# Performance work log

Measured on AMD Instinct MI355X. Metric: run time of the kernel, lower is better.

Reference implementation:

```python
import jax, jax.numpy as jnp
import numpy as np

L, H, LATENT, DM, DH, FF = 4, 4, 256, 768, 192, 1024
EPS = 1e-6      # fast_transformers RecurrentLinearAttention eps
LN_EPS = 1e-5


def make_pe(d_model=LATENT, max_len=5000):
    pos = np.arange(max_len, dtype=np.float32)[:, None]
    div = np.exp(np.arange(0, d_model, 2, dtype=np.float32) * (-np.log(10000.0) / d_model))
    pe = np.zeros((max_len, d_model), np.float32)
    pe[:, 0::2] = np.sin(pos * div)
    pe[:, 1::2] = np.cos(pos * div)
    return jnp.asarray(pe)

PE = make_pe()


def layer_norm(x, g, b):
    m = x.mean(-1, keepdims=True)
    v = ((x - m) ** 2).mean(-1, keepdims=True)
    return (x - m) * jax.lax.rsqrt(v + LN_EPS) * g + b


def setup_inputs() -> dict:
    key = jax.random.key(0)
    ks = jax.random.split(key, 16)
    bs, nj, nf, T, A, C = 8, 25, 6, 80, 6, 12
    s = 0.02
    return dict(
        x=jax.random.normal(ks[0], (bs, nj, nf, T), jnp.float32),
        y=jax.random.randint(ks[1], (bs, A), 0, C),
        ind_map=jnp.sort(jax.random.randint(ks[2], (T, bs), 0, A), axis=0),
        act_tstamps=jnp.sort(jax.random.randint(ks[3], (bs, A), 1, T + 1), axis=1).at[:, -1].set(T),
        skel_W=jax.random.normal(ks[4], (nj * nf, LATENT), jnp.float32) * s,
        skel_b=jnp.zeros((LATENT,), jnp.float32),
        muQuery=jax.random.normal(ks[5], (C, LATENT), jnp.float32),
        sigmaQuery=jax.random.normal(ks[6], (C, LATENT), jnp.float32),
        Wq=jax.random.normal(ks[7], (L, DM, DM), jnp.float32) * s,
        bq=jnp.zeros((L, DM), jnp.float32),
        Wk=jax.random.normal(ks[8], (L, DM, DM), jnp.float32) * s,
        bk=jnp.zeros((L, DM), jnp.float32),
        Wv=jax.random.normal(ks[9], (L, DM, DM), jnp.float32) * s,
        bv=jnp.zeros((L, DM), jnp.float32),
        Wo=jax.random.normal(ks[10], (L, DM, DM), jnp.float32) * s,
        bo=jnp.zeros((L, DM), jnp.float32),
        W1=jax.random.normal(ks[11], (L, DM, FF), jnp.float32) * s,
        b1=jnp.zeros((L, FF), jnp.float32),
        W2=jax.random.normal(ks[12], (L, FF, DM), jnp.float32) * s,
        b2=jnp.zeros((L, DM), jnp.float32),
        ln1_g=jnp.ones((L, DM), jnp.float32), ln1_b=jnp.zeros((L, DM), jnp.float32),
        ln2_g=jnp.ones((L, DM), jnp.float32), ln2_b=jnp.zeros((L, DM), jnp.float32),
        lnf_g=jnp.ones((DM,), jnp.float32), lnf_b=jnp.zeros((DM,), jnp.float32),
    )


def _fwd(x, y, ind_map, act_tstamps, skel_W, skel_b, muQuery, sigmaQuery,
         Wq, bq, Wk, bk, Wv, bv, Wo, bo, W1, b1, W2, b2,
         ln1_g, ln1_b, ln2_g, ln2_b, lnf_g, lnf_b):
    bs, nj, nf, T = x.shape
    # skeleton embedding: [T, bs, njoints*nfeats] @ W -> [T, bs, LATENT]
    xe = x.transpose(3, 0, 1, 2).reshape(T, bs, nj * nf) @ skel_W + skel_b
    mu_q = muQuery[y]        # [bs, A, LATENT]
    sig_q = sigmaQuery[y]
    barange = jnp.arange(bs)

    @jax.checkpoint
    def step(carry, inputs):
        S, Z = carry                         # [L,bs,H,DH,DH], [L,bs,H,DH]
        t, xt, ind_t = inputs
        cm = mu_q[barange, ind_t]            # gather per-sample current action query
        cs = sig_q[barange, ind_t]
        xseq = jnp.stack([cm, cs, xt], 0)    # [3, bs, LATENT]
        start = jnp.where(t == 0, 0, t + 2)  # PositionalEncoding(last_pos=t, offset=2)
        pe3 = jax.lax.dynamic_slice_in_dim(PE, start, 3, 0)
        xseq = xseq + pe3[:, None, :]
        h = xseq.transpose(1, 0, 2).reshape(bs, 3 * LATENT)  # flatten -> [bs, DM]
        nS, nZ = [], []
        for l in range(L):
            q = (h @ Wq[l] + bq[l]).reshape(bs, H, DH)
            k = (h @ Wk[l] + bk[l]).reshape(bs, H, DH)
            v = (h @ Wv[l] + bv[l]).reshape(bs, H, DH)
            Q = jax.nn.elu(q) + 1.0          # linear-attention feature map
            K = jax.nn.elu(k) + 1.0
            Sl = S[l] + K[..., :, None] * v[..., None, :]   # state update S += k (x) v
            Zl = Z[l] + K
            inv = 1.0 / (jnp.einsum('bhd,bhd->bh', Q, Zl) + EPS)
            att = jnp.einsum('bhd,bhdm,bh->bhm', Q, Sl, inv).reshape(bs, DM)
            h1 = layer_norm(h + att @ Wo[l] + bo[l], ln1_g[l], ln1_b[l])
            ffn = jax.nn.relu(h1 @ W1[l] + b1[l]) @ W2[l] + b2[l]
            h = layer_norm(h1 + ffn, ln2_g[l], ln2_b[l])
            nS.append(Sl); nZ.append(Zl)
        h = layer_norm(h, lnf_g, lnf_b)      # encoder final norm
        return (jnp.stack(nS), jnp.stack(nZ)), h

    S0 = jnp.zeros((L, bs, H, DH, DH), x.dtype)
    Z0 = jnp.zeros((L, bs, H, DH), x.dtype)
    _, finals = jax.lax.scan(step, (S0, Z0), (jnp.arange(T), xe, ind_map))  # finals: [T,bs,DM]
    tsel = jnp.maximum(act_tstamps - 1, 0)                       # [bs, A]
    mu = finals[:, :, :LATENT][tsel, barange[:, None]]           # [bs, A, LATENT]
    logvar = finals[:, :, LATENT:2 * LATENT][tsel, barange[:, None]]
    return mu, logvar


def reference(x, y, ind_map, act_tstamps, skel_W, skel_b, muQuery, sigmaQuery,
              Wq, bq, Wk, bk, Wv, bv, Wo, bo, W1, b1, W2, b2,
              ln1_g, ln1_b, ln2_g, ln2_b, lnf_g, lnf_b):
    return _fwd(x, y, ind_map, act_tstamps, skel_W, skel_b, muQuery, sigmaQuery,
                Wq, bq, Wk, bk, Wv, bv, Wo, bo, W1, b1, W2, b2,
                ln1_g, ln1_b, ln2_g, ln2_b, lnf_g, lnf_b)
```

## Files before the change

kernel.cpp:

```cpp
#include <hip/hip_runtime.h>
#include <math.h>

#define TT 80
#define BS 8
#define NA 6
#define DMODEL 768
#define NH 4
#define DH 192
#define FFD 1024
#define NROWS (TT*BS)
#define NQKV (3*DMODEL)

typedef __bf16 bf16;
typedef __bf16 bf16x8 __attribute__((ext_vector_type(8)));
typedef float  f32x4  __attribute__((ext_vector_type(4)));

__device__ __forceinline__ float block_reduce_sum256(float v, float* sm4) {
#pragma unroll
    for (int off = 32; off > 0; off >>= 1) v += __shfl_down(v, off, 64);
    int lane = threadIdx.x & 63, wid = threadIdx.x >> 6;
    if (lane == 0) sm4[wid] = v;
    __syncthreads();
    float r = sm4[0] + sm4[1] + sm4[2] + sm4[3];
    __syncthreads();
    return r;
}

__global__ __launch_bounds__(256) void embed_k(
        const float* __restrict__ x, const int* __restrict__ y,
        const int* __restrict__ ind_map, const float* __restrict__ skel_W,
        const float* __restrict__ skel_b, const float* __restrict__ muQ,
        const float* __restrict__ sigQ, float* __restrict__ h0,
        bf16* __restrict__ h0b) {
    __shared__ float xrow[152];
    int r = blockIdx.x;
    int t = r >> 3, b = r & 7;
    int c = threadIdx.x;
    if (c < 150) xrow[c] = x[(b * 150 + c) * TT + t];
    __syncthreads();
    float acc = skel_b[c];
    for (int jf = 0; jf < 150; jf++) acc += xrow[jf] * skel_W[jf * 256 + c];
    int ind_t = ind_map[t * 8 + b];
    int yb = y[b * NA + ind_t];
    float cm = muQ[yb * 256 + c];
    float cs = sigQ[yb * 256 + c];
    int start = (t == 0) ? 0 : (t + 2);
    float div = expf((float)(c & ~1) * (-9.210340371976184f / 256.0f));
    float p0, p1, p2;
    if (c & 1) {
        p0 = cosf((float)start * div);
        p1 = cosf((float)(start + 1) * div);
        p2 = cosf((float)(start + 2) * div);
    } else {
        p0 = sinf((float)start * div);
        p1 = sinf((float)(start + 1) * div);
        p2 = sinf((float)(start + 2) * div);
    }
    float* hr = h0 + (size_t)r * DMODEL;
    float v0 = cm + p0, v1 = cs + p1, v2 = acc + p2;
    hr[c] = v0; hr[c + 256] = v1; hr[c + 512] = v2;
    bf16* hb = h0b + (size_t)r * DMODEL;
    hb[c] = (bf16)v0; hb[c + 256] = (bf16)v1; hb[c + 512] = (bf16)v2;
}

__global__ __launch_bounds__(256) void transpose_k(
        const float* __restrict__ Wq, const float* __restrict__ Wk,
        const float* __restrict__ Wv, const float* __restrict__ Wo,
        const float* __restrict__ W1, const float* __restrict__ W2,
        bf16* __restrict__ qkvT, bf16* __restrict__ woT,
        bf16* __restrict__ w1T, bf16* __restrict__ w2T) {
    int lz = blockIdx.z;
    int l = lz >> 2, z = lz & 3;
    int K = (z == 3) ? 1024 : 768;
    int N = (z == 0) ? 2304 : (z == 2) ? 1024 : 768;
    int k0 = blockIdx.x * 32, n0 = blockIdx.y * 32;
    if (k0 >= K || n0 >= N) return;
    const float* src; bf16* dst; int ldsrc; int ncol;
    if (z == 0) {
        if (n0 < 768)       { src = Wq + (size_t)l * 768 * 768; ncol = n0; }
        else if (n0 < 1536) { src = Wk + (size_t)l * 768 * 768; ncol = n0 - 768; }
        else                { src = Wv + (size_t)l * 768 * 768; ncol = n0 - 1536; }
        dst = qkvT + (size_t)l * NQKV * DMODEL; ldsrc = 768;
    } else if (z == 1) { src = Wo + (size_t)l * 768 * 768;  dst = woT + (size_t)l * 768 * 768;  ldsrc = 768;  ncol = n0; }
    else if (z == 2)   { src = W1 + (size_t)l * 768 * 1024; dst = w1T + (size_t)l * 1024 * 768; ldsrc = 1024; ncol = n0; }
    else               { src = W2 + (size_t)l * 1024 * 768; dst = w2T + (size_t)l * 768 * 1024; ldsrc = 768;  ncol = n0; }
    __shared__ float tile[32][33];
    int tx = threadIdx.x & 31, ty = threadIdx.x >> 5;
#pragma unroll
    for (int i = 0; i < 4; i++) {
        int r = ty + 8 * i;
        tile[r][tx] = src[(size_t)(k0 + r) * ldsrc + ncol + tx];
    }
    __syncthreads();
#pragma unroll
    for (int i = 0; i < 4; i++) {
        int r = ty + 8 * i;
        dst[(size_t)(n0 + r) * K + k0 + tx] = (bf16)tile[tx][r];
    }
}

template <int EPI>
__global__ __launch_bounds__(256) void gemm_mfma(
        const bf16* __restrict__ A, const bf16* __restrict__ Bt,
        const float* __restrict__ bias_q, const float* __restrict__ bias_k,
        const float* __restrict__ bias_v, const float* __restrict__ resid,
        float* __restrict__ outF, bf16* __restrict__ outB,
        int M, int N, int K) {
    __shared__ __attribute__((aligned(16))) bf16 As0[64][40];
    __shared__ __attribute__((aligned(16))) bf16 As1[64][40];
    __shared__ __attribute__((aligned(16))) bf16 Bs0[64][40];
    __shared__ __attribute__((aligned(16))) bf16 Bs1[64][40];
    int tid = threadIdx.x;
    int m0 = blockIdx.y * 64, n0 = blockIdx.x * 64;
    int w = tid >> 6;
    int l = tid & 63;
    int lm = l & 15, lq = l >> 4;
    int sr = tid >> 2;
    int sk = (tid & 3) * 8;
    const bf16* Arow = &A[(size_t)(m0 + sr) * K];
    const bf16* Brow = &Bt[(size_t)(n0 + sr) * K];
    f32x4 acc[4] = {};
    uint4 a0 = *(const uint4*)&Arow[sk];
    uint4 a1 = *(const uint4*)&Arow[32 + sk];
    uint4 b0 = *(const uint4*)&Brow[sk];
    uint4 b1 = *(const uint4*)&Brow[32 + sk];
    for (int k0 = 0; k0 < K; k0 += 64) {
        __syncthreads();
        *(uint4*)&As0[sr][sk] = a0;
        *(uint4*)&As1[sr][sk] = a1;
        *(uint4*)&Bs0[sr][sk] = b0;
        *(uint4*)&Bs1[sr][sk] = b1;
        __syncthreads();
        int k2 = k0 + 64; if (k2 >= K) k2 = 0;
        a0 = *(const uint4*)&Arow[k2 + sk];
        a1 = *(const uint4*)&Arow[k2 + 32 + sk];
        b0 = *(const uint4*)&Brow[k2 + sk];
        b1 = *(const uint4*)&Brow[k2 + 32 + sk];
        bf16x8 af0 = *(bf16x8*)&As0[w * 16 + lm][lq * 8];
        bf16x8 af1 = *(bf16x8*)&As1[w * 16 + lm][lq * 8];
#pragma unroll
        for (int nb = 0; nb < 4; nb++) {
            bf16x8 bf0 = *(bf16x8*)&Bs0[nb * 16 + lm][lq * 8];
            acc[nb] = __builtin_amdgcn_mfma_f32_16x16x32_bf16(af0, bf0, acc[nb], 0, 0, 0);
        }
#pragma unroll
        for (int nb = 0; nb < 4; nb++) {
            bf16x8 bf1 = *(bf16x8*)&Bs1[nb * 16 + lm][lq * 8];
            acc[nb] = __builtin_amdgcn_mfma_f32_16x16x32_bf16(af1, bf1, acc[nb], 0, 0, 0);
        }
    }
#pragma unroll
    for (int nb = 0; nb < 4; nb++) {
        int col = n0 + nb * 16 + lm;
        float b;
        bool do_elu = false;
        if (EPI == 0) {
            if (col < 768)       { b = bias_q[col];        do_elu = true; }
            else if (col < 1536) { b = bias_k[col - 768];  do_elu = true; }
            else                 { b = bias_v[col - 1536]; }
        } else {
            b = bias_q[col];
        }
#pragma unroll
        for (int r = 0; r < 4; r++) {
            int row = m0 + w * 16 + lq * 4 + r;
            float v = acc[nb][r] + b;
            if (EPI == 0) {
                if (do_elu) v = (v > 0.0f) ? (v + 1.0f) : expf(v);
                outB[(size_t)row * N + col] = (bf16)v;
            } else if (EPI == 1) {
                v += resid[(size_t)row * N + col];
                outF[(size_t)row * N + col] = v;
            } else {
                v = fmaxf(v, 0.0f);
                outB[(size_t)row * N + col] = (bf16)v;
            }
        }
    }
}

__global__ __launch_bounds__(256) void ln_k(
        const float* __restrict__ in, float* __restrict__ outF,
        bf16* __restrict__ outB,
        const float* __restrict__ g, const float* __restrict__ b) {
    int wave = threadIdx.x >> 6, lane = threadIdx.x & 63;
    int row = blockIdx.x * 4 + wave;
    const float* xr = in + (size_t)row * DMODEL;
    float4 v[3];
    float s = 0.0f;
#pragma unroll
    for (int j = 0; j < 3; j++) {
        v[j] = *(const float4*)&xr[lane * 4 + 256 * j];
        s += v[j].x + v[j].y + v[j].z + v[j].w;
    }
#pragma unroll
    for (int mk = 1; mk < 64; mk <<= 1) s += __shfl_xor(s, mk, 64);
    float m = s * (1.0f / 768.0f);
    float sq = 0.0f;
#pragma unroll
    for (int j = 0; j < 3; j++) {
        v[j].x -= m; v[j].y -= m; v[j].z -= m; v[j].w -= m;
        sq += v[j].x * v[j].x + v[j].y * v[j].y + v[j].z * v[j].z + v[j].w * v[j].w;
    }
#pragma unroll
    for (int mk = 1; mk < 64; mk <<= 1) sq += __shfl_xor(sq, mk, 64);
    float r = rsqrtf(sq * (1.0f / 768.0f) + 1e-5f);
    float* orow = outF + (size_t)row * DMODEL;
    bf16* brow = outB + (size_t)row * DMODEL;
#pragma unroll
    for (int j = 0; j < 3; j++) {
        int c = lane * 4 + 256 * j;
        float4 gg = *(const float4*)&g[c];
        float4 bb = *(const float4*)&b[c];
        float o0 = v[j].x * r * gg.x + bb.x;
        float o1 = v[j].y * r * gg.y + bb.y;
        float o2 = v[j].z * r * gg.z + bb.z;
        float o3 = v[j].w * r * gg.w + bb.w;
        *(float4*)&orow[c] = make_float4(o0, o1, o2, o3);
        bf16 tmp4[4] = {(bf16)o0, (bf16)o1, (bf16)o2, (bf16)o3};
        *(uint2*)&brow[c] = *(uint2*)tmp4;
    }
}

__global__ __launch_bounds__(320) void attn_k(
        const bf16* __restrict__ qkvB, bf16* __restrict__ att) {
    __shared__ __attribute__((aligned(16))) char smem[64000];
    bf16* Qs = (bf16*)smem;
    bf16* Ks = (bf16*)(smem + 32000);
    bf16* Aij = (bf16*)smem;
    bf16* VT = (bf16*)(smem + 16640);

    int b = blockIdx.x >> 2, h = blockIdx.x & 3;
    int tid = threadIdx.x;
    int w = tid >> 6, l = tid & 63;
    int lm = l & 15, lq = l >> 4;

    uint4 vreg[6];
#pragma unroll
    for (int u = 0; u < 6; u++) {
        int c = tid + 320 * u;
        int t = c / 24, cc = c % 24;
        int d0 = cc * 8;
        size_t g = (size_t)(t * 8 + b) * NQKV + h * DH + d0;
        uint4 qv = *(const uint4*)&qkvB[g];
        uint4 kv = *(const uint4*)&qkvB[g + 768];
        vreg[u]  = *(const uint4*)&qkvB[g + 1536];
        *(uint4*)&Qs[t * 200 + d0] = qv;
        *(uint4*)&Ks[t * 200 + d0] = kv;
    }
    __syncthreads();

    f32x4 acc[5] = {};
#pragma unroll
    for (int k0 = 0; k0 < 192; k0 += 32) {
        bf16x8 af = *(bf16x8*)&Qs[(w * 16 + lm) * 200 + lq * 8 + k0];
#pragma unroll
        for (int nb = 0; nb < 5; nb++) {
            bf16x8 bfr = *(bf16x8*)&Ks[(nb * 16 + lm) * 200 + lq * 8 + k0];
            acc[nb] = __builtin_amdgcn_mfma_f32_16x16x32_bf16(af, bfr, acc[nb], 0, 0, 0);
        }
    }
    float mval[5][4];
    float rs[4] = {0.f, 0.f, 0.f, 0.f};
#pragma unroll
    for (int nb = 0; nb < 5; nb++)
#pragma unroll
        for (int r = 0; r < 4; r++) {
            int t = w * 16 + lq * 4 + r, tau = nb * 16 + lm;
            float v = (tau <= t) ? acc[nb][r] : 0.0f;
            mval[nb][r] = v;
            rs[r] += v;
        }
#pragma unroll
    for (int mk = 1; mk < 16; mk <<= 1)
#pragma unroll
        for (int r = 0; r < 4; r++) rs[r] += __shfl_xor(rs[r], mk, 64);
    float inv[4];
#pragma unroll
    for (int r = 0; r < 4; r++) inv[r] = 1.0f / (rs[r] + 1e-6f);

    __syncthreads();

#pragma unroll
    for (int nb = 0; nb < 5; nb++)
#pragma unroll
        for (int r = 0; r < 4; r++)
            Aij[(w * 16 + lq * 4 + r) * 104 + nb * 16 + lm] = (bf16)mval[nb][r];
    *(uint2*)&Aij[(tid >> 2) * 104 + 80 + (tid & 3) * 4] = make_uint2(0u, 0u);
#pragma unroll
    for (int u = 0; u < 6; u++) {
        int c = tid + 320 * u;
        int t = c / 24, cc = c % 24;
        int d0 = cc * 8;
        bf16 tmp8[8];
        *(uint4*)tmp8 = vreg[u];
#pragma unroll
        for (int j = 0; j < 8; j++) VT[(d0 + j) * 104 + t] = tmp8[j];
    }
    if (tid < 192) {
        *(uint4*)&VT[tid * 104 + 80] = make_uint4(0u, 0u, 0u, 0u);
        *(uint4*)&VT[tid * 104 + 88] = make_uint4(0u, 0u, 0u, 0u);
    }
    __syncthreads();

#pragma unroll 1
    for (int nc = 0; nc < 12; nc++) {
        f32x4 a2 = {};
#pragma unroll
        for (int k0 = 0; k0 < 96; k0 += 32) {
            bf16x8 af = *(bf16x8*)&Aij[(w * 16 + lm) * 104 + lq * 8 + k0];
            bf16x8 bfr = *(bf16x8*)&VT[(nc * 16 + lm) * 104 + lq * 8 + k0];
            a2 = __builtin_amdgcn_mfma_f32_16x16x32_bf16(af, bfr, a2, 0, 0, 0);
        }
#pragma unroll
        for (int r = 0; r < 4; r++) {
            int t = w * 16 + lq * 4 + r;
            att[(size_t)(t * 8 + b) * DMODEL + h * DH + nc * 16 + lm] =
                (bf16)(a2[r] * inv[r]);
        }
    }
}

__global__ __launch_bounds__(256) void final_k(
        const float* __restrict__ h, const int* __restrict__ act_ts,
        const float* __restrict__ g, const float* __restrict__ bb,
        float* __restrict__ out) {
    __shared__ float sm4[4];
    int ba = blockIdx.x;
    int b = ba / NA;
    int ts = act_ts[ba];
    int t = ts - 1; if (t < 0) t = 0;
    const float* xr = h + (size_t)(t * 8 + b) * DMODEL;
    int c = threadIdx.x;
    float x0 = xr[c], x1 = xr[c + 256], x2 = xr[c + 512];
    float m = block_reduce_sum256(x0 + x1 + x2, sm4) * (1.0f / 768.0f);
    float d0 = x0 - m, d1 = x1 - m, d2 = x2 - m;
    float v = block_reduce_sum256(d0 * d0 + d1 * d1 + d2 * d2, sm4) * (1.0f / 768.0f);
    float r = rsqrtf(v + 1e-5f);
    out[ba * 256 + c]            = d0 * r * g[c] + bb[c];
    out[48 * 256 + ba * 256 + c] = d1 * r * g[c + 256] + bb[c + 256];
}

extern "C" void kernel_launch(void* const* d_in, const int* in_sizes, int n_in,
                              void* d_out, int out_size, void* d_ws, size_t ws_size,
                              hipStream_t stream) {
    const float* x       = (const float*)d_in[0];
    const int*   y       = (const int*)d_in[1];
    const int*   ind_map = (const int*)d_in[2];
    const int*   act_ts  = (const int*)d_in[3];
    const float* skel_W  = (const float*)d_in[4];
    const float* skel_b  = (const float*)d_in[5];
    const float* muQ     = (const float*)d_in[6];
    const float* sigQ    = (const float*)d_in[7];
    const float* Wq = (const float*)d_in[8];   const float* bq = (const float*)d_in[9];
    const float* Wk = (const float*)d_in[10];  const float* bk = (const float*)d_in[11];
    const float* Wv = (const float*)d_in[12];  const float* bv = (const float*)d_in[13];
    const float* Wo = (const float*)d_in[14];  const float* bo = (const float*)d_in[15];
    const float* W1 = (const float*)d_in[16];  const float* b1 = (const float*)d_in[17];
    const float* W2 = (const float*)d_in[18];  const float* b2 = (const float*)d_in[19];
    const float* ln1_g = (const float*)d_in[20]; const float* ln1_b = (const float*)d_in[21];
    const float* ln2_g = (const float*)d_in[22]; const float* ln2_b = (const float*)d_in[23];
    const float* lnf_g = (const float*)d_in[24]; const float* lnf_b = (const float*)d_in[25];
    float* out = (float*)d_out;

    char* p = (char*)d_ws;
    const size_t R  = (size_t)NROWS * DMODEL;
    float* h    = (float*)p; p += R * 4;
    float* h1   = (float*)p; p += R * 4;
    float* tmp  = (float*)p; p += R * 4;
    bf16* qkvB  = (bf16*)p;  p += (size_t)NROWS * NQKV * 2;
    bf16* hB    = (bf16*)p;  p += R * 2;
    bf16* h1B   = (bf16*)p;  p += R * 2;
    bf16* attB  = (bf16*)p;  p += R * 2;
    bf16* ffn1B = (bf16*)p;  p += (size_t)NROWS * FFD * 2;
    bf16* qkvT  = (bf16*)p;  p += (size_t)4 * NQKV * DMODEL * 2;
    bf16* woT   = (bf16*)p;  p += (size_t)4 * DMODEL * DMODEL * 2;
    bf16* w1T   = (bf16*)p;  p += (size_t)4 * FFD * DMODEL * 2;
    bf16* w2T   = (bf16*)p;  p += (size_t)4 * DMODEL * FFD * 2;

    dim3 gT(32, 72, 16);
    transpose_k<<<gT, 256, 0, stream>>>(Wq, Wk, Wv, Wo, W1, W2, qkvT, woT, w1T, w2T);
    embed_k<<<NROWS, 256, 0, stream>>>(x, y, ind_map, skel_W, skel_b, muQ, sigQ, h, hB);

    dim3 gQKV(NQKV / 64, 10);
    dim3 g768(12, 10);
    dim3 g1024(16, 10);
    for (int l = 0; l < 4; l++) {
        const bf16* qkvTl = qkvT + (size_t)l * NQKV * DMODEL;
        const bf16* woTl  = woT  + (size_t)l * DMODEL * DMODEL;
        const bf16* w1Tl  = w1T  + (size_t)l * FFD * DMODEL;
        const bf16* w2Tl  = w2T  + (size_t)l * DMODEL * FFD;
        gemm_mfma<0><<<gQKV, 256, 0, stream>>>(hB, qkvTl,
                bq + l * DMODEL, bk + l * DMODEL, bv + l * DMODEL,
                nullptr, nullptr, qkvB, NROWS, NQKV, DMODEL);
        attn_k<<<32, 320, 0, stream>>>(qkvB, attB);
        gemm_mfma<1><<<g768, 256, 0, stream>>>(attB, woTl,
                bo + l * DMODEL, nullptr, nullptr, h, tmp, nullptr,
                NROWS, DMODEL, DMODEL);
        ln_k<<<NROWS / 4, 256, 0, stream>>>(tmp, h1, h1B, ln1_g + l * DMODEL, ln1_b + l * DMODEL);
        gemm_mfma<2><<<g1024, 256, 0, stream>>>(h1B, w1Tl,
                b1 + l * FFD, nullptr, nullptr, nullptr, nullptr, ffn1B,
                NROWS, FFD, DMODEL);
        gemm_mfma<1><<<g768, 256, 0, stream>>>(ffn1B, w2Tl,
                b2 + l * DMODEL, nullptr, nullptr, h1, tmp, nullptr,
                NROWS, DMODEL, FFD);
        ln_k<<<NROWS / 4, 256, 0, stream>>>(tmp, h, hB, ln2_g + l * DMODEL, ln2_b + l * DMODEL);
    }

    final_k<<<48, 256, 0, stream>>>(h, act_ts, lnf_g, lnf_b, out);
}
```

Before: 423.6 us.

## Fuse LayerNorm into GEMM prologue/epilogue via atomic row stats; merge prep kernels

Removes the standalone LayerNorm kernels. The residual GEMM epilogue now accumulates each row's sum and sum-of-squares with atomics, and the next GEMM normalizes its fp32 A operand on the fly, or normalizes the residual in its epilogue. The weight transpose and embedding are merged into one prep kernel that also zeroes the stats buffer. Attention is split across three blocks per batch-head to raise parallelism. This trades fewer launches and fewer round trips to memory for fp32 A loads in the fused GEMMs, a single-pass variance formula that is less numerically stable, and duplicated QK work in attention.

After: 441.2 us. 4.1% more time.

```diff
diff --git a/kernel.cpp b/kernel.cpp
--- a/kernel.cpp
+++ b/kernel.cpp
@@ -5,15 +5,368 @@
 #define BS 8
 #define NA 6
 #define DMODEL 768
-#define NH 4
 #define DH 192
 #define FFD 1024
-#define NROWS (TT*BS)
-#define NQKV (3*DMODEL)
+#define NROWS 640
+#define NQKV 2304
 
 typedef __bf16 bf16;
 typedef __bf16 bf16x8 __attribute__((ext_vector_type(8)));
 typedef float  f32x4  __attribute__((ext_vector_type(4)));
+
+__device__ __forceinline__ void row_ms(const float* __restrict__ st, int row,
+                                       float& m, float& rs) {
+    float s1 = st[row * 2], s2 = st[row * 2 + 1];
+    m = s1 * (1.0f / 768.0f);
+    float var = s2 * (1.0f / 768.0f) - m * m;
+    rs = rsqrtf(var + 1e-5f);
+}
+
+struct TJob { const float* src; bf16* dst; int ldsrc, Kd, n0, k0; };
+
+__global__ __launch_bounds__(256) void prep_k(
+        const float* __restrict__ x, const int* __restrict__ y,
+        const int* __restrict__ ind_map,
+        const float* __restrict__ skel_W, const float* __restrict__ skel_b,
+        const float* __restrict__ muQ, const float* __restrict__ sigQ,
+        const float* __restrict__ Wq, const float* __restrict__ Wk,
+        const float* __restrict__ Wv, const float* __restrict__ Wo,
+        const float* __restrict__ W1, const float* __restrict__ W2,
+        bf16* __restrict__ qkvT, bf16* __restrict__ woT,
+        bf16* __restrict__ w1T, bf16* __restrict__ w2T,
+        float* __restrict__ h, bf16* __restrict__ h0B,
+        float* __restrict__ stats) {
+    __shared__ float tile[32][33];
+    __shared__ float xrow[152];
+    int bid = blockIdx.x, tid = threadIdx.x;
+    if (bid < 15360) {
+        TJob J;
+        int l = bid / 3840, r = bid % 3840;
+        if (r < 1728) {
+            int kt = r % 24, nt = r / 24;
+            J.k0 = kt * 32; J.n0 = nt * 32; J.Kd = 768; J.ldsrc = 768;
+            J.dst = qkvT + (size_t)l * NQKV * DMODEL;
+            if (J.n0 < 768)       { J.src = Wq + (size_t)l * 589824 + J.n0; }
+            else if (J.n0 < 1536) { J.src = Wk + (size_t)l * 589824 + (J.n0 - 768); }
+            else                  { J.src = Wv + (size_t)l * 589824 + (J.n0 - 1536); }
+        } else if (r < 2304) {
+            int r2 = r - 1728; int kt = r2 % 24, nt = r2 / 24;
+            J.k0 = kt * 32; J.n0 = nt * 32; J.Kd = 768; J.ldsrc = 768;
+            J.src = Wo + (size_t)l * 589824 + J.n0;
+            J.dst = woT + (size_t)l * 589824;
+        } else if (r < 3072) {
+            int r2 = r - 2304; int kt = r2 % 24, nt = r2 / 24;
+            J.k0 = kt * 32; J.n0 = nt * 32; J.Kd = 768; J.ldsrc = 1024;
+            J.src = W1 + (size_t)l * 786432 + J.n0;
+            J.dst = w1T + (size_t)l * 786432;
+        } else {
+            int r2 = r - 3072; int kt = r2 % 32, nt = r2 / 32;
+            J.k0 = kt * 32; J.n0 = nt * 32; J.Kd = 1024; J.ldsrc = 768;
+            J.src = W2 + (size_t)l * 786432 + J.n0;
+            J.dst = w2T + (size_t)l * 786432;
+        }
+        int tx = tid & 31, ty = tid >> 5;
+#pragma unroll
+        for (int i = 0; i < 4; i++) {
+            int rr = ty + 8 * i;
+            tile[rr][tx] = J.src[(size_t)(J.k0 + rr) * J.ldsrc + tx];
+        }
+        __syncthreads();
+#pragma unroll
+        for (int i = 0; i < 4; i++) {
+            int rr = ty + 8 * i;
+            J.dst[(size_t)(J.n0 + rr) * J.Kd + J.k0 + tx] = (bf16)tile[tx][rr];
+        }
+    } else {
+        int r = bid - 15360;
+        int t = r >> 3, b = r & 7;
+        int c = tid;
+        if (c < 16) {
+            int arr = c >> 3, l = (c >> 1) & 3, j = c & 1;
+            stats[arr * 5120 + l * 1280 + r * 2 + j] = 0.0f;
+        }
+        if (c < 150) xrow[c] = x[(b * 150 + c) * TT + t];
+        __syncthreads();
+        float acc = skel_b[c];
+        for (int jf = 0; jf < 150; jf++) acc += xrow[jf] * skel_W[jf * 256 + c];
+        int ind_t = ind_map[t * 8 + b];
+        int yb = y[b * NA + ind_t];
+        float cm = muQ[yb * 256 + c];
+        float cs = sigQ[yb * 256 + c];
+        int start = (t == 0) ? 0 : (t + 2);
+        float div = expf((float)(c & ~1) * (-9.210340371976184f / 256.0f));
+        float p0, p1, p2;
+        if (c & 1) {
+            p0 = cosf((float)start * div);
+            p1 = cosf((float)(start + 1) * div);
+            p2 = cosf((float)(start + 2) * div);
+        } else {
+            p0 = sinf((float)start * div);
+            p1 = sinf((float)(start + 1) * div);
+            p2 = sinf((float)(start + 2) * div);
+        }
+        float* hr = h + (size_t)r * DMODEL;
+        float v0 = cm + p0, v1 = cs + p1, v2 = acc + p2;
+        hr[c] = v0; hr[c + 256] = v1; hr[c + 512] = v2;
+        bf16* hb = h0B + (size_t)r * DMODEL;
+        hb[c] = (bf16)v0; hb[c + 256] = (bf16)v1; hb[c + 512] = (bf16)v2;
+    }
+}
+
+template <int EPI, int ANORM, int RNORM>
+__global__ __launch_bounds__(256) void gemm_mfma(
+        const bf16* __restrict__ Ab, const float* __restrict__ Af,
+        const float* __restrict__ stA, const float* __restrict__ gA,
+        const float* __restrict__ bA,
+        const bf16* __restrict__ Bt,
+        const float* __restrict__ bias_q, const float* __restrict__ bias_k,
+        const float* __restrict__ bias_v,
+        const float* __restrict__ residF, const float* __restrict__ stR,
+        const float* __restrict__ gR, const float* __restrict__ bR,
+        float* __restrict__ outF, bf16* __restrict__ outB,
+        float* __restrict__ stOut, int N, int K) {
+    __shared__ __attribute__((aligned(16))) bf16 As0[64][40];
+    __shared__ __attribute__((aligned(16))) bf16 As1[64][40];
+    __shared__ __attribute__((aligned(16))) bf16 Bs0[64][40];
+    __shared__ __attribute__((aligned(16))) bf16 Bs1[64][40];
+    int tid = threadIdx.x;
+    int m0 = blockIdx.y * 64, n0 = blockIdx.x * 64;
+    int w = tid >> 6, l = tid & 63;
+    int lm = l & 15, lq = l >> 4;
+    int sr = tid >> 2;
+    int sk = (tid & 3) * 8;
+    int arow = m0 + sr;
+    const bf16* Brow = &Bt[(size_t)(n0 + sr) * K];
+    f32x4 acc[4] = {};
+    const bf16* Abrow = nullptr; const float* Afrow = nullptr;
+    float mA = 0.f, rsA = 0.f;
+    if (ANORM) {
+        Afrow = &Af[(size_t)arow * K];
+        row_ms(stA, arow, mA, rsA);
+    } else {
+        Abrow = &Ab[(size_t)arow * K];
+    }
+    uint4 a0, a1;
+    f32x4 ax0a, ax0b, ax1a, ax1b;
+    if (ANORM) {
+        ax0a = *(const f32x4*)&Afrow[sk];      ax0b = *(const f32x4*)&Afrow[sk + 4];
+        ax1a = *(const f32x4*)&Afrow[32 + sk]; ax1b = *(const f32x4*)&Afrow[36 + sk];
+    } else {
+        a0 = *(const uint4*)&Abrow[sk];
+        a1 = *(const uint4*)&Abrow[32 + sk];
+    }
+    uint4 b0 = *(const uint4*)&Brow[sk];
+    uint4 b1 = *(const uint4*)&Brow[32 + sk];
+    for (int k0 = 0; k0 < K; k0 += 64) {
+        __syncthreads();
+        if (ANORM) {
+            union { bf16 t[8]; uint4 u; } c0, c1;
+            const float* gp = gA + k0 + sk;
+            const float* bp = bA + k0 + sk;
+#pragma unroll
+            for (int j = 0; j < 4; j++) {
+                c0.t[j]     = (bf16)((ax0a[j] - mA) * rsA * gp[j]      + bp[j]);
+                c0.t[j + 4] = (bf16)((ax0b[j] - mA) * rsA * gp[j + 4]  + bp[j + 4]);
+                c1.t[j]     = (bf16)((ax1a[j] - mA) * rsA * gp[32 + j] + bp[32 + j]);
+                c1.t[j + 4] = (bf16)((ax1b[j] - mA) * rsA * gp[36 + j] + bp[36 + j]);
+            }
+            *(uint4*)&As0[sr][sk] = c0.u;
+            *(uint4*)&As1[sr][sk] = c1.u;
+        } else {
+            *(uint4*)&As0[sr][sk] = a0;
+            *(uint4*)&As1[sr][sk] = a1;
+        }
+        *(uint4*)&Bs0[sr][sk] = b0;
+        *(uint4*)&Bs1[sr][sk] = b1;
+        __syncthreads();
+        int k2 = k0 + 64; if (k2 >= K) k2 = 0;
+        if (ANORM) {
+            ax0a = *(const f32x4*)&Afrow[k2 + sk];      ax0b = *(const f32x4*)&Afrow[k2 + sk + 4];
+            ax1a = *(const f32x4*)&Afrow[k2 + 32 + sk]; ax1b = *(const f32x4*)&Afrow[k2 + 36 + sk];
+        } else {
+            a0 = *(const uint4*)&Abrow[k2 + sk];
+            a1 = *(const uint4*)&Abrow[k2 + 32 + sk];
+        }
+        b0 = *(const uint4*)&Brow[k2 + sk];
+        b1 = *(const uint4*)&Brow[k2 + 32 + sk];
+        bf16x8 af0 = *(bf16x8*)&As0[w * 16 + lm][lq * 8];
+        bf16x8 af1 = *(bf16x8*)&As1[w * 16 + lm][lq * 8];
+#pragma unroll
+        for (int nb = 0; nb < 4; nb++) {
+            bf16x8 bfr = *(bf16x8*)&Bs0[nb * 16 + lm][lq * 8];
+            acc[nb] = __builtin_amdgcn_mfma_f32_16x16x32_bf16(af0, bfr, acc[nb], 0, 0, 0);
+        }
+#pragma unroll
+        for (int nb = 0; nb < 4; nb++) {
+            bf16x8 bfr = *(bf16x8*)&Bs1[nb * 16 + lm][lq * 8];
+            acc[nb] = __builtin_amdgcn_mfma_f32_16x16x32_bf16(af1, bfr, acc[nb], 0, 0, 0);
+        }
+    }
+    if (EPI == 1) {
+        float mR4[4], rsR4[4];
+        if (RNORM) {
+#pragma unroll
+            for (int r = 0; r < 4; r++)
+                row_ms(stR, m0 + w * 16 + lq * 4 + r, mR4[r], rsR4[r]);
+        }
+        float s1[4] = {0.f, 0.f, 0.f, 0.f}, s2[4] = {0.f, 0.f, 0.f, 0.f};
+#pragma unroll
+        for (int nb = 0; nb < 4; nb++) {
+            int col = n0 + nb * 16 + lm;
+            float bia = bias_q[col];
+            float gc = 0.f, bc = 0.f;
+            if (RNORM) { gc = gR[col]; bc = bR[col]; }
+#pragma unroll
+            for (int r = 0; r < 4; r++) {
+                int row = m0 + w * 16 + lq * 4 + r;
+                float rv = residF[(size_t)row * N + col];
+                if (RNORM) rv = (rv - mR4[r]) * rsR4[r] * gc + bc;
+                float v = acc[nb][r] + bia + rv;
+                outF[(size_t)row * N + col] = v;
+                s1[r] += v; s2[r] += v * v;
+            }
+        }
+#pragma unroll
+        for (int mk = 1; mk < 16; mk <<= 1) {
+#pragma unroll
+            for (int r = 0; r < 4; r++) {
+                s1[r] += __shfl_xor(s1[r], mk, 64);
+                s2[r] += __shfl_xor(s2[r], mk, 64);
+            }
+        }
+        if (lm == 0) {
+#pragma unroll
+            for (int r = 0; r < 4; r++) {
+                int row = m0 + w * 16 + lq * 4 + r;
+                atomicAdd(&stOut[row * 2],     s1[r]);
+                atomicAdd(&stOut[row * 2 + 1], s2[r]);
+            }
+        }
+    } else {
+#pragma unroll
+        for (int nb = 0; nb < 4; nb++) {
+            int col = n0 + nb * 16 + lm;
+            float bia; bool do_elu = false;
+            if (EPI == 0) {
+                if (col < 768)       { bia = bias_q[col];        do_elu = true; }
+                else if (col < 1536) { bia = bias_k[col - 768];  do_elu = true; }
+                else                 { bia = bias_v[col - 1536]; }
+            } else {
+                bia = bias_q[col];
+            }
+#pragma unroll
+            for (int r = 0; r < 4; r++) {
+                int row = m0 + w * 16 + lq * 4 + r;
+                float v = acc[nb][r] + bia;
+                if (EPI == 0) {
+                    if (do_elu) v = (v > 0.0f) ? (v + 1.0f) : expf(v);
+                    outB[(size_t)row * N + col] = (bf16)v;
+                } else {
+                    outB[(size_t)row * N + col] = (bf16)fmaxf(v, 0.0f);
+                }
+            }
+        }
+    }
+}
+
+__global__ __launch_bounds__(320) void attn_k(
+        const bf16* __restrict__ qkvB, bf16* __restrict__ att) {
+    __shared__ __attribute__((aligned(16))) char smem[64000];
+    bf16* Qs = (bf16*)smem;
+    bf16* Ks = (bf16*)(smem + 32000);
+    bf16* Aij = (bf16*)smem;
+    bf16* VT = (bf16*)(smem + 16640);
+    int bh = blockIdx.x / 3, part = blockIdx.x % 3;
+    int bb = bh >> 2, hd = bh & 3;
+    int tid = threadIdx.x;
+    int w = tid >> 6, l = tid & 63;
+    int lm = l & 15, lq = l >> 4;
+
+    uint4 vreg[6];
+#pragma unroll
+    for (int u = 0; u < 6; u++) {
+        int c = tid + 320 * u;
+        int t = c / 24, cc = c % 24;
+        int d0 = cc * 8;
+        size_t g = (size_t)(t * 8 + bb) * NQKV + hd * DH + d0;
+        uint4 qv = *(const uint4*)&qkvB[g];
+        uint4 kv = *(const uint4*)&qkvB[g + 768];
+        vreg[u]  = *(const uint4*)&qkvB[g + 1536];
+        *(uint4*)&Qs[t * 200 + d0] = qv;
+        *(uint4*)&Ks[t * 200 + d0] = kv;
+    }
+    __syncthreads();
+
+    f32x4 acc[5] = {};
+#pragma unroll
+    for (int k0 = 0; k0 < 192; k0 += 32) {
+        bf16x8 af = *(bf16x8*)&Qs[(w * 16 + lm) * 200 + lq * 8 + k0];
+#pragma unroll
+        for (int nb = 0; nb < 5; nb++) {
+            bf16x8 bfr = *(bf16x8*)&Ks[(nb * 16 + lm) * 200 + lq * 8 + k0];
+            acc[nb] = __builtin_amdgcn_mfma_f32_16x16x32_bf16(af, bfr, acc[nb], 0, 0, 0);
+        }
+    }
+    float mval[5][4];
+    float rs[4] = {0.f, 0.f, 0.f, 0.f};
+#pragma unroll
+    for (int nb = 0; nb < 5; nb++)
+#pragma unroll
+        for (int r = 0; r < 4; r++) {
+            int t = w * 16 + lq * 4 + r, tau = nb * 16 + lm;
+            float v = (tau <= t) ? acc[nb][r] : 0.0f;
+            mval[nb][r] = v;
+            rs[r] += v;
+        }
+#pragma unroll
+    for (int mk = 1; mk < 16; mk <<= 1)
+#pragma unroll
+        for (int r = 0; r < 4; r++) rs[r] += __shfl_xor(rs[r], mk, 64);
+    float inv[4];
+#pragma unroll
+    for (int r = 0; r < 4; r++) inv[r] = 1.0f / (rs[r] + 1e-6f);
+
+    __syncthreads();
+
+#pragma unroll
+    for (int nb = 0; nb < 5; nb++)
+#pragma unroll
+        for (int r = 0; r < 4; r++)
+            Aij[(w * 16 + lq * 4 + r) * 104 + nb * 16 + lm] = (bf16)mval[nb][r];
+    *(uint2*)&Aij[(tid >> 2) * 104 + 80 + (tid & 3) * 4] = make_uint2(0u, 0u);
+#pragma unroll
+    for (int u = 0; u < 6; u++) {
+        int c = tid + 320 * u;
+        int t = c / 24, cc = c % 24;
+        int d0 = cc * 8;
+        bf16 tmp8[8];
+        *(uint4*)tmp8 = vreg[u];
+#pragma unroll
+        for (int j = 0; j < 8; j++) VT[(d0 + j) * 104 + t] = tmp8[j];
+    }
+    if (tid < 192) {
+        *(uint4*)&VT[tid * 104 + 80] = make_uint4(0u, 0u, 0u, 0u);
+        *(uint4*)&VT[tid * 104 + 88] = make_uint4(0u, 0u, 0u, 0u);
+    }
+    __syncthreads();
+
+#pragma unroll 1
+    for (int nc = part * 4; nc < part * 4 + 4; nc++) {
+        f32x4 a2 = {};
+#pragma unroll
+        for (int k0 = 0; k0 < 96; k0 += 32) {
+            bf16x8 af = *(bf16x8*)&Aij[(w * 16 + lm) * 104 + lq * 8 + k0];
+            bf16x8 bfr = *(bf16x8*)&VT[(nc * 16 + lm) * 104 + lq * 8 + k0];
+            a2 = __builtin_amdgcn_mfma_f32_16x16x32_bf16(af, bfr, a2, 0, 0, 0);
+        }
+#pragma unroll
+        for (int r = 0; r < 4; r++) {
+            int t = w * 16 + lq * 4 + r;
+            att[(size_t)(t * 8 + bb) * DMODEL + hd * DH + nc * 16 + lm] =
+                (bf16)(a2[r] * inv[r]);
+        }
+    }
+}
 
 __device__ __forceinline__ float block_reduce_sum256(float v, float* sm4) {
 #pragma unroll
@@ -26,319 +379,31 @@
     return r;
 }
 
-__global__ __launch_bounds__(256) void embed_k(
-        const float* __restrict__ x, const int* __restrict__ y,
-        const int* __restrict__ ind_map, const float* __restrict__ skel_W,
-        const float* __restrict__ skel_b, const float* __restrict__ muQ,
-        const float* __restrict__ sigQ, float* __restrict__ h0,
-        bf16* __restrict__ h0b) {
-    __shared__ float xrow[152];
-    int r = blockIdx.x;
-    int t = r >> 3, b = r & 7;
-    int c = threadIdx.x;
-    if (c < 150) xrow[c] = x[(b * 150 + c) * TT + t];
-    __syncthreads();
-    float acc = skel_b[c];
-    for (int jf = 0; jf < 150; jf++) acc += xrow[jf] * skel_W[jf * 256 + c];
-    int ind_t = ind_map[t * 8 + b];
-    int yb = y[b * NA + ind_t];
-    float cm = muQ[yb * 256 + c];
-    float cs = sigQ[yb * 256 + c];
-    int start = (t == 0) ? 0 : (t + 2);
-    float div = expf((float)(c & ~1) * (-9.210340371976184f / 256.0f));
-    float p0, p1, p2;
-    if (c & 1) {
-        p0 = cosf((float)start * div);
-        p1 = cosf((float)(start + 1) * div);
-        p2 = cosf((float)(start + 2) * div);
-    } else {
-        p0 = sinf((float)start * div);
-        p1 = sinf((float)(start + 1) * div);
-        p2 = sinf((float)(start + 2) * div);
-    }
-    float* hr = h0 + (size_t)r * DMODEL;
-    float v0 = cm + p0, v1 = cs + p1, v2 = acc + p2;
-    hr[c] = v0; hr[c + 256] = v1; hr[c + 512] = v2;
-    bf16* hb = h0b + (size_t)r * DMODEL;
-    hb[c] = (bf16)v0; hb[c + 256] = (bf16)v1; hb[c + 512] = (bf16)v2;
-}
-
-__global__ __launch_bounds__(256) void transpose_k(
-        const float* __restrict__ Wq, const float* __restrict__ Wk,
-        const float* __restrict__ Wv, const float* __restrict__ Wo,
-        const float* __restrict__ W1, const float* __restrict__ W2,
-        bf16* __restrict__ qkvT, bf16* __restrict__ woT,
-        bf16* __restrict__ w1T, bf16* __restrict__ w2T) {
-    int lz = blockIdx.z;
-    int l = lz >> 2, z = lz & 3;
-    int K = (z == 3) ? 1024 : 768;
-    int N = (z == 0) ? 2304 : (z == 2) ? 1024 : 768;
-    int k0 = blockIdx.x * 32, n0 = blockIdx.y * 32;
-    if (k0 >= K || n0 >= N) return;
-    const float* src; bf16* dst; int ldsrc; int ncol;
-    if (z == 0) {
-        if (n0 < 768)       { src = Wq + (size_t)l * 768 * 768; ncol = n0; }
-        else if (n0 < 1536) { src = Wk + (size_t)l * 768 * 768; ncol = n0 - 768; }
-        else                { src = Wv + (size_t)l * 768 * 768; ncol = n0 - 1536; }
-        dst = qkvT + (size_t)l * NQKV * DMODEL; ldsrc = 768;
-    } else if (z == 1) { src = Wo + (size_t)l * 768 * 768;  dst = woT + (size_t)l * 768 * 768;  ldsrc = 768;  ncol = n0; }
-    else if (z == 2)   { src = W1 + (size_t)l * 768 * 1024; dst = w1T + (size_t)l * 1024 * 768; ldsrc = 1024; ncol = n0; }
-    else               { src = W2 + (size_t)l * 1024 * 768; dst = w2T + (size_t)l * 768 * 1024; ldsrc = 768;  ncol = n0; }
-    __shared__ float tile[32][33];
-    int tx = threadIdx.x & 31, ty = threadIdx.x >> 5;
-#pragma unroll
-    for (int i = 0; i < 4; i++) {
-        int r = ty + 8 * i;
-        tile[r][tx] = src[(size_t)(k0 + r) * ldsrc + ncol + tx];
-    }
-    __syncthreads();
-#pragma unroll
-    for (int i = 0; i < 4; i++) {
-        int r = ty + 8 * i;
-        dst[(size_t)(n0 + r) * K + k0 + tx] = (bf16)tile[tx][r];
-    }
-}
-
-template <int EPI>
-__global__ __launch_bounds__(256) void gemm_mfma(
-        const bf16* __restrict__ A, const bf16* __restrict__ Bt,
-        const float* __restrict__ bias_q, const float* __restrict__ bias_k,
-        const float* __restrict__ bias_v, const float* __restrict__ resid,
-        float* __restrict__ outF, bf16* __restrict__ outB,
-        int M, int N, int K) {
-    __shared__ __attribute__((aligned(16))) bf16 As0[64][40];
-    __shared__ __attribute__((aligned(16))) bf16 As1[64][40];
-    __shared__ __attribute__((aligned(16))) bf16 Bs0[64][40];
-    __shared__ __attribute__((aligned(16))) bf16 Bs1[64][40];
-    int tid = threadIdx.x;
-    int m0 = blockIdx.y * 64, n0 = blockIdx.x * 64;
-    int w = tid >> 6;
-    int l = tid & 63;
-    int lm = l & 15, lq = l >> 4;
-    int sr = tid >> 2;
-    int sk = (tid & 3) * 8;
-    const bf16* Arow = &A[(size_t)(m0 + sr) * K];
-    const bf16* Brow = &Bt[(size_t)(n0 + sr) * K];
-    f32x4 acc[4] = {};
-    uint4 a0 = *(const uint4*)&Arow[sk];
-    uint4 a1 = *(const uint4*)&Arow[32 + sk];
-    uint4 b0 = *(const uint4*)&Brow[sk];
-    uint4 b1 = *(const uint4*)&Brow[32 + sk];
-    for (int k0 = 0; k0 < K; k0 += 64) {
-        __syncthreads();
-        *(uint4*)&As0[sr][sk] = a0;
-        *(uint4*)&As1[sr][sk] = a1;
-        *(uint4*)&Bs0[sr][sk] = b0;
-        *(uint4*)&Bs1[sr][sk] = b1;
-        __syncthreads();
-        int k2 = k0 + 64; if (k2 >= K) k2 = 0;
-        a0 = *(const uint4*)&Arow[k2 + sk];
-        a1 = *(const uint4*)&Arow[k2 + 32 + sk];
-        b0 = *(const uint4*)&Brow[k2 + sk];
-        b1 = *(const uint4*)&Brow[k2 + 32 + sk];
-        bf16x8 af0 = *(bf16x8*)&As0[w * 16 + lm][lq * 8];
-        bf16x8 af1 = *(bf16x8*)&As1[w * 16 + lm][lq * 8];
-#pragma unroll
-        for (int nb = 0; nb < 4; nb++) {
-            bf16x8 bf0 = *(bf16x8*)&Bs0[nb * 16 + lm][lq * 8];
-            acc[nb] = __builtin_amdgcn_mfma_f32_16x16x32_bf16(af0, bf0, acc[nb], 0, 0, 0);
-        }
-#pragma unroll
-        for (int nb = 0; nb < 4; nb++) {
-            bf16x8 bf1 = *(bf16x8*)&Bs1[nb * 16 + lm][lq * 8];
-            acc[nb] = __builtin_amdgcn_mfma_f32_16x16x32_bf16(af1, bf1, acc[nb], 0, 0, 0);
-        }
-    }
-#pragma unroll
-    for (int nb = 0; nb < 4; nb++) {
-        int col = n0 + nb * 16 + lm;
-        float b;
-        bool do_elu = false;
-        if (EPI == 0) {
-            if (col < 768)       { b = bias_q[col];        do_elu = true; }
-            else if (col < 1536) { b = bias_k[col - 768];  do_elu = true; }
-            else                 { b = bias_v[col - 1536]; }
-        } else {
-            b = bias_q[col];
-        }
-#pragma unroll
-        for (int r = 0; r < 4; r++) {
-            int row = m0 + w * 16 + lq * 4 + r;
-            float v = acc[nb][r] + b;
-            if (EPI == 0) {
-                if (do_elu) v = (v > 0.0f) ? (v + 1.0f) : expf(v);
-                outB[(size_t)row * N + col] = (bf16)v;
-            } else if (EPI == 1) {
-                v += resid[(size_t)row * N + col];
-                outF[(size_t)row * N + col] = v;
-            } else {
-                v = fmaxf(v, 0.0f);
-                outB[(size_t)row * N + col] = (bf16)v;
-            }
-        }
-    }
-}
-
-__global__ __launch_bounds__(256) void ln_k(
-        const float* __restrict__ in, float* __restrict__ outF,
-        bf16* __restrict__ outB,
-        const float* __restrict__ g, const float* __restrict__ b) {
-    int wave = threadIdx.x >> 6, lane = threadIdx.x & 63;
-    int row = blockIdx.x * 4 + wave;
-    const float* xr = in + (size_t)row * DMODEL;
-    float4 v[3];
-    float s = 0.0f;
-#pragma unroll
-    for (int j = 0; j < 3; j++) {
-        v[j] = *(const float4*)&xr[lane * 4 + 256 * j];
-        s += v[j].x + v[j].y + v[j].z + v[j].w;
-    }
-#pragma unroll
-    for (int mk = 1; mk < 64; mk <<= 1) s += __shfl_xor(s, mk, 64);
-    float m = s * (1.0f / 768.0f);
-    float sq = 0.0f;
-#pragma unroll
-    for (int j = 0; j < 3; j++) {
-        v[j].x -= m; v[j].y -= m; v[j].z -= m; v[j].w -= m;
-        sq += v[j].x * v[j].x + v[j].y * v[j].y + v[j].z * v[j].z + v[j].w * v[j].w;
-    }
-#pragma unroll
-    for (int mk = 1; mk < 64; mk <<= 1) sq += __shfl_xor(sq, mk, 64);
-    float r = rsqrtf(sq * (1.0f / 768.0f) + 1e-5f);
-    float* orow = outF + (size_t)row * DMODEL;
-    bf16* brow = outB + (size_t)row * DMODEL;
-#pragma unroll
-    for (int j = 0; j < 3; j++) {
-        int c = lane * 4 + 256 * j;
-        float4 gg = *(const float4*)&g[c];
-        float4 bb = *(const float4*)&b[c];
-        float o0 = v[j].x * r * gg.x + bb.x;
-        float o1 = v[j].y * r * gg.y + bb.y;
-        float o2 = v[j].z * r * gg.z + bb.z;
-        float o3 = v[j].w * r * gg.w + bb.w;
-        *(float4*)&orow[c] = make_float4(o0, o1, o2, o3);
-        bf16 tmp4[4] = {(bf16)o0, (bf16)o1, (bf16)o2, (bf16)o3};
-        *(uint2*)&brow[c] = *(uint2*)tmp4;
-    }
-}
-
-__global__ __launch_bounds__(320) void attn_k(
-        const bf16* __restrict__ qkvB, bf16* __restrict__ att) {
-    __shared__ __attribute__((aligned(16))) char smem[64000];
-    bf16* Qs = (bf16*)smem;
-    bf16* Ks = (bf16*)(smem + 32000);
-    bf16* Aij = (bf16*)smem;
-    bf16* VT = (bf16*)(smem + 16640);
-
-    int b = blockIdx.x >> 2, h = blockIdx.x & 3;
-    int tid = threadIdx.x;
-    int w = tid >> 6, l = tid & 63;
-    int lm = l & 15, lq = l >> 4;
-
-    uint4 vreg[6];
-#pragma unroll
-    for (int u = 0; u < 6; u++) {
-        int c = tid + 320 * u;
-        int t = c / 24, cc = c % 24;
-        int d0 = cc * 8;
-        size_t g = (size_t)(t * 8 + b) * NQKV + h * DH + d0;
-        uint4 qv = *(const uint4*)&qkvB[g];
-        uint4 kv = *(const uint4*)&qkvB[g + 768];
-        vreg[u]  = *(const uint4*)&qkvB[g + 1536];
-        *(uint4*)&Qs[t * 200 + d0] = qv;
-        *(uint4*)&Ks[t * 200 + d0] = kv;
-    }
-    __syncthreads();
-
-    f32x4 acc[5] = {};
-#pragma unroll
-    for (int k0 = 0; k0 < 192; k0 += 32) {
-        bf16x8 af = *(bf16x8*)&Qs[(w * 16 + lm) * 200 + lq * 8 + k0];
-#pragma unroll
-        for (int nb = 0; nb < 5; nb++) {
-            bf16x8 bfr = *(bf16x8*)&Ks[(nb * 16 + lm) * 200 + lq * 8 + k0];
-            acc[nb] = __builtin_amdgcn_mfma_f32_16x16x32_bf16(af, bfr, acc[nb], 0, 0, 0);
-        }
-    }
-    float mval[5][4];
-    float rs[4] = {0.f, 0.f, 0.f, 0.f};
-#pragma unroll
-    for (int nb = 0; nb < 5; nb++)
-#pragma unroll
-        for (int r = 0; r < 4; r++) {
-            int t = w * 16 + lq * 4 + r, tau = nb * 16 + lm;
-            float v = (tau <= t) ? acc[nb][r] : 0.0f;
-            mval[nb][r] = v;
-            rs[r] += v;
-        }
-#pragma unroll
-    for (int mk = 1; mk < 16; mk <<= 1)
-#pragma unroll
-        for (int r = 0; r < 4; r++) rs[r] += __shfl_xor(rs[r], mk, 64);
-    float inv[4];
-#pragma unroll
-    for (int r = 0; r < 4; r++) inv[r] = 1.0f / (rs[r] + 1e-6f);
-
-    __syncthreads();
-
-#pragma unroll
-    for (int nb = 0; nb < 5; nb++)
-#pragma unroll
-        for (int r = 0; r < 4; r++)
-            Aij[(w * 16 + lq * 4 + r) * 104 + nb * 16 + lm] = (bf16)mval[nb][r];
-    *(uint2*)&Aij[(tid >> 2) * 104 + 80 + (tid & 3) * 4] = make_uint2(0u, 0u);
-#pragma unroll
-    for (int u = 0; u < 6; u++) {
-        int c = tid + 320 * u;
-        int t = c / 24, cc = c % 24;
-        int d0 = cc * 8;
-        bf16 tmp8[8];
-        *(uint4*)tmp8 = vreg[u];
-#pragma unroll
-        for (int j = 0; j < 8; j++) VT[(d0 + j) * 104 + t] = tmp8[j];
-    }
-    if (tid < 192) {
-        *(uint4*)&VT[tid * 104 + 80] = make_uint4(0u, 0u, 0u, 0u);
-        *(uint4*)&VT[tid * 104 + 88] = make_uint4(0u, 0u, 0u, 0u);
-    }
-    __syncthreads();
-
-#pragma unroll 1
-    for (int nc = 0; nc < 12; nc++) {
-        f32x4 a2 = {};
-#pragma unroll
-        for (int k0 = 0; k0 < 96; k0 += 32) {
-            bf16x8 af = *(bf16x8*)&Aij[(w * 16 + lm) * 104 + lq * 8 + k0];
-            bf16x8 bfr = *(bf16x8*)&VT[(nc * 16 + lm) * 104 + lq * 8 + k0];
-            a2 = __builtin_amdgcn_mfma_f32_16x16x32_bf16(af, bfr, a2, 0, 0, 0);
-        }
-#pragma unroll
-        for (int r = 0; r < 4; r++) {
-            int t = w * 16 + lq * 4 + r;
-            att[(size_t)(t * 8 + b) * DMODEL + h * DH + nc * 16 + lm] =
-                (bf16)(a2[r] * inv[r]);
-        }
-    }
-}
-
 __global__ __launch_bounds__(256) void final_k(
-        const float* __restrict__ h, const int* __restrict__ act_ts,
-        const float* __restrict__ g, const float* __restrict__ bb,
+        const float* __restrict__ tmp2, const float* __restrict__ st2,
+        const float* __restrict__ g2, const float* __restrict__ b2,
+        const int* __restrict__ act_ts,
+        const float* __restrict__ gf, const float* __restrict__ bf_,
         float* __restrict__ out) {
     __shared__ float sm4[4];
     int ba = blockIdx.x;
     int b = ba / NA;
     int ts = act_ts[ba];
     int t = ts - 1; if (t < 0) t = 0;
-    const float* xr = h + (size_t)(t * 8 + b) * DMODEL;
+    int row = t * 8 + b;
+    const float* xr = tmp2 + (size_t)row * DMODEL;
     int c = threadIdx.x;
-    float x0 = xr[c], x1 = xr[c + 256], x2 = xr[c + 512];
+    float m2, rs2;
+    row_ms(st2, row, m2, rs2);
+    float x0 = (xr[c]       - m2) * rs2 * g2[c]       + b2[c];
+    float x1 = (xr[c + 256] - m2) * rs2 * g2[c + 256] + b2[c + 256];
+    float x2 = (xr[c + 512] - m2) * rs2 * g2[c + 512] + b2[c + 512];
     float m = block_reduce_sum256(x0 + x1 + x2, sm4) * (1.0f / 768.0f);
     float d0 = x0 - m, d1 = x1 - m, d2 = x2 - m;
     float v = block_reduce_sum256(d0 * d0 + d1 * d1 + d2 * d2, sm4) * (1.0f / 768.0f);
     float r = rsqrtf(v + 1e-5f);
-    out[ba * 256 + c]            = d0 * r * g[c] + bb[c];
-    out[48 * 256 + ba * 256 + c] = d1 * r * g[c + 256] + bb[c + 256];
+    out[ba * 256 + c]            = d0 * r * gf[c] + bf_[c];
+    out[48 * 256 + ba * 256 + c] = d1 * r * gf[c + 256] + bf_[c + 256];
 }
 
 extern "C" void kernel_launch(void* const* d_in, const int* in_sizes, int n_in,
@@ -364,23 +429,23 @@
     float* out = (float*)d_out;
 
     char* p = (char*)d_ws;
-    const size_t R  = (size_t)NROWS * DMODEL;
-    float* h    = (float*)p; p += R * 4;
-    float* h1   = (float*)p; p += R * 4;
-    float* tmp  = (float*)p; p += R * 4;
-    bf16* qkvB  = (bf16*)p;  p += (size_t)NROWS * NQKV * 2;
-    bf16* hB    = (bf16*)p;  p += R * 2;
-    bf16* h1B   = (bf16*)p;  p += R * 2;
-    bf16* attB  = (bf16*)p;  p += R * 2;
-    bf16* ffn1B = (bf16*)p;  p += (size_t)NROWS * FFD * 2;
-    bf16* qkvT  = (bf16*)p;  p += (size_t)4 * NQKV * DMODEL * 2;
-    bf16* woT   = (bf16*)p;  p += (size_t)4 * DMODEL * DMODEL * 2;
-    bf16* w1T   = (bf16*)p;  p += (size_t)4 * FFD * DMODEL * 2;
-    bf16* w2T   = (bf16*)p;  p += (size_t)4 * DMODEL * FFD * 2;
-
-    dim3 gT(32, 72, 16);
-    transpose_k<<<gT, 256, 0, stream>>>(Wq, Wk, Wv, Wo, W1, W2, qkvT, woT, w1T, w2T);
-    embed_k<<<NROWS, 256, 0, stream>>>(x, y, ind_map, skel_W, skel_b, muQ, sigQ, h, hB);
+    const size_t R = (size_t)NROWS * DMODEL;
+    float* h     = (float*)p; p += R * 4;
+    float* tmp1  = (float*)p; p += R * 4;
+    float* tmp2  = (float*)p; p += R * 4;
+    float* stats = (float*)p; p += 10240 * 4;
+    bf16* h0B    = (bf16*)p;  p += R * 2;
+    bf16* qkvB   = (bf16*)p;  p += (size_t)NROWS * NQKV * 2;
+    bf16* attB   = (bf16*)p;  p += R * 2;
+    bf16* ffn1B  = (bf16*)p;  p += (size_t)NROWS * FFD * 2;
+    bf16* qkvT   = (bf16*)p;  p += (size_t)4 * NQKV * DMODEL * 2;
+    bf16* woT    = (bf16*)p;  p += (size_t)4 * DMODEL * DMODEL * 2;
+    bf16* w1T    = (bf16*)p;  p += (size_t)4 * FFD * DMODEL * 2;
+    bf16* w2T    = (bf16*)p;  p += (size_t)4 * DMODEL * FFD * 2;
+
+    prep_k<<<16000, 256, 0, stream>>>(x, y, ind_map, skel_W, skel_b, muQ, sigQ,
+                                      Wq, Wk, Wv, Wo, W1, W2,
+                                      qkvT, woT, w1T, w2T, h, h0B, stats);
 
     dim3 gQKV(NQKV / 64, 10);
     dim3 g768(12, 10);
@@ -390,22 +455,54 @@
         const bf16* woTl  = woT  + (size_t)l * DMODEL * DMODEL;
         const bf16* w1Tl  = w1T  + (size_t)l * FFD * DMODEL;
         const bf16* w2Tl  = w2T  + (size_t)l * DMODEL * FFD;
-        gemm_mfma<0><<<gQKV, 256, 0, stream>>>(hB, qkvTl,
+        float* st1 = stats + l * 1280;
+        float* st2 = stats + 5120 + l * 1280;
+        const float* st2p = stats + 5120 + (l - 1) * 1280;
+        const float* g2p = ln2_g + (l - 1) * DMODEL;
+        const float* b2p = ln2_b + (l - 1) * DMODEL;
+
+        if (l == 0)
+            gemm_mfma<0, 0, 0><<<gQKV, 256, 0, stream>>>(
+                h0B, nullptr, nullptr, nullptr, nullptr, qkvTl,
+                bq, bk, bv,
+                nullptr, nullptr, nullptr, nullptr,
+                nullptr, qkvB, nullptr, NQKV, DMODEL);
+        else
+            gemm_mfma<0, 1, 0><<<gQKV, 256, 0, stream>>>(
+                nullptr, tmp2, st2p, g2p, b2p, qkvTl,
                 bq + l * DMODEL, bk + l * DMODEL, bv + l * DMODEL,
-                nullptr, nullptr, qkvB, NROWS, NQKV, DMODEL);
-        attn_k<<<32, 320, 0, stream>>>(qkvB, attB);
-        gemm_mfma<1><<<g768, 256, 0, stream>>>(attB, woTl,
-                bo + l * DMODEL, nullptr, nullptr, h, tmp, nullptr,
-                NROWS, DMODEL, DMODEL);
-        ln_k<<<NROWS / 4, 256, 0, stream>>>(tmp, h1, h1B, ln1_g + l * DMODEL, ln1_b + l * DMODEL);
-        gemm_mfma<2><<<g1024, 256, 0, stream>>>(h1B, w1Tl,
-                b1 + l * FFD, nullptr, nullptr, nullptr, nullptr, ffn1B,
-                NROWS, FFD, DMODEL);
-        gemm_mfma<1><<<g768, 256, 0, stream>>>(ffn1B, w2Tl,
-                b2 + l * DMODEL, nullptr, nullptr, h1, tmp, nullptr,
-                NROWS, DMODEL, FFD);
-        ln_k<<<NROWS / 4, 256, 0, stream>>>(tmp, h, hB, ln2_g + l * DMODEL, ln2_b + l * DMODEL);
-    }
-
-    final_k<<<48, 256, 0, stream>>>(h, act_ts, lnf_g, lnf_b, out);
-}
+                nullptr, nullptr, nullptr, nullptr,
+                nullptr, qkvB, nullptr, NQKV, DMODEL);
+
+        attn_k<<<96, 320, 0, stream>>>(qkvB, attB);
+
+        if (l == 0)
+            gemm_mfma<1, 0, 0><<<g768, 256, 0, stream>>>(
+                attB, nullptr, nullptr, nullptr, nullptr, woTl,
+                bo, nullptr, nullptr,
+                h, nullptr, nullptr, nullptr,
+                tmp1, nullptr, st1, DMODEL, DMODEL);
+        else
+            gemm_mfma<1, 0, 1><<<g768, 256, 0, stream>>>(
+                attB, nullptr, nullptr, nullptr, nullptr, woTl,
+                bo + l * DMODEL, nullptr, nullptr,
+                tmp2, st2p, g2p, b2p,
+                tmp1, nullptr, st1, DMODEL, DMODEL);
+
+        gemm_mfma<2, 1, 0><<<g1024, 256, 0, stream>>>(
+            nullptr, tmp1, st1, ln1_g + l * DMODEL, ln1_b + l * DMODEL, w1Tl,
+            b1 + l * FFD, nullptr, nullptr,
+            nullptr, nullptr, nullptr, nullptr,
+            nullptr, ffn1B, nullptr, FFD, DMODEL);
+
+        gemm_mfma<1, 0, 1><<<g768, 256, 0, stream>>>(
+            ffn1B, nullptr, nullptr, nullptr, nullptr, w2Tl,
+            b2 + l * DMODEL, nullptr, nullptr,
+            tmp1, st1, ln1_g + l * DMODEL, ln1_b + l * DMODEL,
+            tmp2, nullptr, st2, DMODEL, FFD);
+    }
+
+    final_k<<<48, 256, 0, stream>>>(tmp2, stats + 5120 + 3 * 1280,
+                                    ln2_g + 3 * DMODEL, ln2_b + 3 * DMODEL,
+                                    act_ts, lnf_g, lnf_b, out);
+}
```
